# Performance work log

Hardware: AMD Instinct MI355X
Metric: run time of the kernel (lower is better)

## Reference

```python
import jax, jax.numpy as jnp
import numpy as np

B, S, D = 4, 8192, 768
H, HD = 12, 64
CS, NL = 512, 32


def setup_inputs() -> dict:
    key = jax.random.key(0)
    ks = jax.random.split(key, 9)
    sc = 0.02
    return {
        "x": jax.random.normal(ks[0], (B, S, D), jnp.float32),
        "q_w": jax.random.normal(ks[1], (D, D), jnp.float32) * sc,
        "q_b": jax.random.normal(ks[2], (D,), jnp.float32) * sc,
        "k_w": jax.random.normal(ks[3], (D, D), jnp.float32) * sc,
        "k_b": jax.random.normal(ks[4], (D,), jnp.float32) * sc,
        "v_w": jax.random.normal(ks[5], (D, D), jnp.float32) * sc,
        "v_b": jax.random.normal(ks[6], (D,), jnp.float32) * sc,
        "o_w": jax.random.normal(ks[7], (D, D), jnp.float32) * sc,
        "o_b": jax.random.normal(ks[8], (D,), jnp.float32) * sc,
    }


def reference(x, q_w, q_b, k_w, k_b, v_w, v_b, o_w, o_b):
    # x: (B, S, D); S divisible by CS and NL -> no padding / trimming needed.
    scale = HD ** -0.5
    n_chunks = S // CS
    seg = S // NL
    # Global landmarks: mean-pool NL evenly spaced segments. (B, NL, D)
    landmarks = x.reshape(B, NL, seg, D).mean(axis=2)
    # Q only over local tokens (torch Linear: x @ W^T + b)
    q = (x @ q_w.T + q_b).reshape(B, n_chunks, CS, H, HD)
    x_chunks = x.reshape(B, n_chunks, CS, D)
    # Prepend landmarks to every chunk's KV context: ctx = NL + CS
    lm = jnp.broadcast_to(landmarks[:, None], (B, n_chunks, NL, D))
    kv_ctx = jnp.concatenate([lm, x_chunks], axis=2)  # (B, n_chunks, ctx, D)
    ctx = NL + CS
    k = (kv_ctx @ k_w.T + k_b).reshape(B, n_chunks, ctx, H, HD)
    v = (kv_ctx @ v_w.T + v_b).reshape(B, n_chunks, ctx, H, HD)
    scores = jnp.einsum("bnqhd,bnkhd->bnhqk", q, k) * scale
    attn = jax.nn.softmax(scores, axis=-1)  # dropout=0 (eval)
    out = jnp.einsum("bnhqk,bnkhd->bnqhd", attn, v).reshape(B, S, D)
    return out @ o_w.T + o_b
```

## Files before the change

### kernel.cpp

```cpp
#include <hip/hip_runtime.h>


typedef unsigned short u16;
typedef __attribute__((ext_vector_type(8))) short short8;
typedef __attribute__((ext_vector_type(8))) unsigned short u16x8;
typedef __attribute__((ext_vector_type(4))) float f32x4;

__device__ __forceinline__ u16 f2bf(float f) {
    unsigned u = __float_as_uint(f);
    u += 0x7fffu + ((u >> 16) & 1u);
    return (u16)(u >> 16);
}

#define MFMA_BF16(A, B, C) __builtin_amdgcn_mfma_f32_16x16x32_bf16((A), (B), (C), 0, 0, 0)

__device__ __forceinline__ void gload16(const u16* g, const short* l) {
    __builtin_amdgcn_global_load_lds(
        (__attribute__((address_space(1))) void*)g,
        (__attribute__((address_space(3))) void*)l, 16, 0, 0);
}

__global__ __launch_bounds__(256) void k_cvtx(const float* __restrict__ x,
                                              u16* __restrict__ xa,
                                              float* __restrict__ part) {
    const int g = blockIdx.x;
    const int t = threadIdx.x;
    const float* base = x + (size_t)g * 64 * 768;
    u16* ob = xa + (size_t)g * 64 * 768;
    float s0 = 0.f, s1 = 0.f, s2 = 0.f;
    for (int r = 0; r < 64; ++r) {
        const size_t off = (size_t)r * 768;
        const float v0 = base[off + t], v1 = base[off + t + 256], v2 = base[off + t + 512];
        s0 += v0; s1 += v1; s2 += v2;
        ob[off + t] = f2bf(v0); ob[off + t + 256] = f2bf(v1); ob[off + t + 512] = f2bf(v2);
    }
    float* p = part + (size_t)g * 768;
    p[t] = s0; p[t + 256] = s1; p[t + 512] = s2;
}

__global__ void k_lmred(const float* __restrict__ part, u16* __restrict__ xa_lm) {
    const int bl = blockIdx.x;
    const int t = threadIdx.x;
    const float* p = part + (size_t)bl * 4 * 768;
    const float inv = 1.f / 256.f;
    for (int c = t; c < 768; c += 256) {
        const float s = p[c] + p[768 + c] + p[1536 + c] + p[2304 + c];
        xa_lm[(size_t)bl * 768 + c] = f2bf(s * inv);
    }
}

__global__ void k_cvtw(const float* __restrict__ qw, const float* __restrict__ kw,
                       const float* __restrict__ vw, const float* __restrict__ ow,
                       const float* __restrict__ qb, const float* __restrict__ kb,
                       const float* __restrict__ vb,
                       u16* __restrict__ wcat, u16* __restrict__ owb,
                       float* __restrict__ bcat) {
    const int yy = blockIdx.y;
    const int i = blockIdx.x * 256 + threadIdx.x;
    if (yy == 4) {
        if (i < 768)       bcat[i] = qb[i];
        else if (i < 1536) bcat[i] = kb[i - 768];
        else if (i < 2304) bcat[i] = vb[i - 1536];
        return;
    }
    const float* src = (yy == 0) ? qw : (yy == 1) ? kw : (yy == 2) ? vw : ow;
    u16* dst = (yy == 3) ? owb : wcat + (size_t)yy * 589824;
    const float4 v = ((const float4*)src)[i];
    ushort4 o;
    o.x = f2bf(v.x); o.y = f2bf(v.y); o.z = f2bf(v.z); o.w = f2bf(v.w);
    ((ushort4*)dst)[i] = o;
}

template <int MODE>
__global__ __launch_bounds__(256) void k_gemm(
    const u16* __restrict__ A, const u16* __restrict__ Bw, const float* __restrict__ bias,
    u16* __restrict__ q, u16* __restrict__ ktok, u16* __restrict__ vtok,
    u16* __restrict__ klm, u16* __restrict__ vlm, float* __restrict__ outf)
{
    __shared__ short lA[128 * 64];
    __shared__ short lB[128 * 64];
    const int t = threadIdx.x;
    const int wid = t >> 6, l = t & 63, lr = l & 15, lg = l >> 4;
    const int wm = wid >> 1, wn = wid & 1;

    const int gx = gridDim.x;
    const int nwg = gx * gridDim.y;
    const int orig = blockIdx.x + gx * blockIdx.y;
    const int qq = nwg >> 3, rr = nwg & 7, xcd = orig & 7, ii = orig >> 3;
    const int wg = (xcd < rr ? xcd * (qq + 1) : rr * (qq + 1) + (xcd - rr) * qq) + ii;
    const int m0 = (wg / gx) * 128, n0 = (wg % gx) * 128;

    const int srow = t >> 3;
    const int scol = (t & 7) * 8;
    const u16* ga = A  + (size_t)(m0 + srow) * 768 + scol;
    const u16* gb = Bw + (size_t)(n0 + srow) * 768 + scol;
    const int lbase = wid * 8 * 64;

    f32x4 acc[4][4] = {};

    for (int kt = 0; kt < 12; ++kt) {
        const int k0 = kt * 64;
        __syncthreads();
#pragma unroll
        for (int i = 0; i < 4; ++i) {
            gload16(ga + (size_t)(i * 32) * 768 + k0, &lA[i * 32 * 64 + lbase]);
            gload16(gb + (size_t)(i * 32) * 768 + k0, &lB[i * 32 * 64 + lbase]);
        }
        __syncthreads();
#pragma unroll
        for (int kf = 0; kf < 2; ++kf) {
            short8 af[4], bf2[4];
#pragma unroll
            for (int x = 0; x < 4; ++x) {
                af[x]  = *(const short8*)&lA[(wm * 64 + x * 16 + lr) * 64 + kf * 32 + lg * 8];
                bf2[x] = *(const short8*)&lB[(wn * 64 + x * 16 + lr) * 64 + kf * 32 + lg * 8];
            }
#pragma unroll
            for (int mf = 0; mf < 4; ++mf)
#pragma unroll
                for (int nf = 0; nf < 4; ++nf)
                    acc[mf][nf] = MFMA_BF16(af[mf], bf2[nf], acc[mf][nf]);
        }
    }

    if (MODE == 0) {
        const bool is_lm = (m0 >= 32768);
#pragma unroll
        for (int nf = 0; nf < 4; ++nf) {
            const int gn = n0 + wn * 64 + nf * 16 + lr;
            const float bv = bias[gn];
            const int region = gn / 768;
            const int nn = gn - region * 768;
            const int h = nn >> 6, d = nn & 63;
            u16* dst  = (region == 0) ? q : (region == 1) ? ktok : vtok;
            u16* dstl = (region == 1) ? klm : vlm;
#pragma unroll
            for (int mf = 0; mf < 4; ++mf) {
                const int gmb = m0 + wm * 64 + mf * 16 + lg * 4;
#pragma unroll
                for (int r = 0; r < 4; ++r) {
                    const u16 val = f2bf(acc[mf][nf][r] + bv);
                    const int gm = gmb + r;
                    if (!is_lm) {
                        const int b = gm >> 13, s = gm & 8191;
                        dst[((size_t)(b * 12 + h) * 8192 + s) * 64 + d] = val;
                    } else if (region > 0) {
                        const int ii2 = gm - 32768;
                        const int b = ii2 >> 5, lmr = ii2 & 31;
                        dstl[((size_t)(b * 12 + h) * 32 + lmr) * 64 + d] = val;
                    }
                }
            }
        }
    } else {
#pragma unroll
        for (int nf = 0; nf < 4; ++nf) {
            const int gn = n0 + wn * 64 + nf * 16 + lr;
            const float bv = bias[gn];
#pragma unroll
            for (int mf = 0; mf < 4; ++mf) {
                const int gmb = m0 + wm * 64 + mf * 16 + lg * 4;
#pragma unroll
                for (int r = 0; r < 4; ++r)
                    outf[(size_t)(gmb + r) * 768 + gn] = acc[mf][nf][r] + bv;
            }
        }
    }
}

__global__ __launch_bounds__(256) void k_tv(const u16* __restrict__ vtok, u16* __restrict__ vt) {
    __shared__ u16 tl[64 * 72];
    const int t = threadIdx.x;
    const int bh = blockIdx.x >> 7;
    const int s0 = (blockIdx.x & 127) * 64;
#pragma unroll
    for (int i = 0; i < 2; ++i) {
        const int qq = t + 256 * i;
        const int s = qq >> 3, c = qq & 7;
        *(uint4*)&tl[s * 72 + c * 8] =
            *(const uint4*)(vtok + ((size_t)bh * 8192 + s0 + s) * 64 + c * 8);
    }
    __syncthreads();
    const int d = t >> 2, sc = t & 3;
    u16x8 a, b2;
#pragma unroll
    for (int j = 0; j < 8; ++j) a[j] = tl[(sc * 16 + j) * 72 + d];
#pragma unroll
    for (int j = 0; j < 8; ++j) b2[j] = tl[(sc * 16 + 8 + j) * 72 + d];
    u16* o = vt + ((size_t)bh * 64 + d) * 8192 + s0 + sc * 16;
    *(u16x8*)(o) = a;
    *(u16x8*)(o + 8) = b2;
}

__global__ void k_tvlm(const u16* __restrict__ vlm, u16* __restrict__ vlmt) {
    const int e = blockIdx.x * 256 + threadIdx.x;
    if (e >= 98304) return;
    const int bh = e >> 11, rem = e & 2047, d = rem >> 5, lm = rem & 31;
    vlmt[(size_t)bh * 2048 + d * 32 + lm] = vlm[(size_t)bh * 2048 + lm * 64 + d];
}

__global__ __launch_bounds__(256) void k_attn(
    const u16* __restrict__ q, const u16* __restrict__ ktok,
    const u16* __restrict__ klm, const u16* __restrict__ vt,
    const u16* __restrict__ vlmt, u16* __restrict__ ao)
{
    __shared__ short kls[2][32 * 72];
    __shared__ short vls[2][64 * 40];
    __shared__ short pls[4][64 * 40];
    const int t = threadIdx.x, wid = t >> 6, l = t & 63, lr = l & 15, lg = l >> 4;
    const int idx = blockIdx.x;
    const int qt = idx & 1;
    const int h  = (idx >> 1) % 12;
    const int cb = (idx >> 1) / 12;
    const int c  = cb & 15, b = cb >> 4;
    const int bh = b * 12 + h;
    const int sb = c * 512 + qt * 256 + wid * 64;

    short8 qf[4][2];
#pragma unroll
    for (int mf = 0; mf < 4; ++mf)
#pragma unroll
        for (int kf = 0; kf < 2; ++kf)
            qf[mf][kf] = *(const short8*)(q + ((size_t)bh * 8192 + sb + mf * 16 + lr) * 64
                                            + kf * 32 + lg * 8);

    f32x4 O[4][4] = {};
    float lsum[4][4] = {};

    short* pw = &pls[wid][0];
    const int kn = t >> 3, kko = (t & 7) * 8;
    const int kctx = (kn < 16) ? (kn * 2) : ((kn - 16) * 2 + 1);
    const int vd = t >> 2, vco = (t & 3) * 8;

    auto kaddr = [&](int ti) -> const u16* {
        if (ti == 0) return klm + ((size_t)bh * 32 + kctx) * 64 + kko;
        return ktok + ((size_t)bh * 8192 + c * 512 + (ti - 1) * 32 + kctx) * 64 + kko;
    };
    auto vaddr = [&](int ti) -> const u16* {
        if (ti == 0) return vlmt + ((size_t)bh * 64 + vd) * 32 + vco;
        return vt + ((size_t)bh * 64 + vd) * 8192 + c * 512 + (ti - 1) * 32 + vco;
    };

    {
        const uint4 rk0 = *(const uint4*)kaddr(0);
        const uint4 rv0 = *(const uint4*)vaddr(0);
        *(uint4*)&kls[0][kn * 72 + kko] = rk0;
        *(uint4*)&vls[0][vd * 40 + vco] = rv0;
    }
    __syncthreads();

    for (int ti = 0; ti < 17; ++ti) {
        const int cur = ti & 1, nxt = cur ^ 1;
        uint4 rk, rv;
        if (ti < 16) { rk = *(const uint4*)kaddr(ti + 1); rv = *(const uint4*)vaddr(ti + 1); }

        f32x4 sc[4][2] = {};
#pragma unroll
        for (int kf = 0; kf < 2; ++kf) {
            const short8 b0 = *(const short8*)&kls[cur][(lr)      * 72 + kf * 32 + lg * 8];
            const short8 b1 = *(const short8*)&kls[cur][(16 + lr) * 72 + kf * 32 + lg * 8];
#pragma unroll
            for (int mf = 0; mf < 4; ++mf) {
                sc[mf][0] = MFMA_BF16(qf[mf][kf], b0, sc[mf][0]);
                sc[mf][1] = MFMA_BF16(qf[mf][kf], b1, sc[mf][1]);
            }
        }

#pragma unroll
        for (int mf = 0; mf < 4; ++mf) {
#pragma unroll
            for (int r = 0; r < 4; ++r) {
                const float p0 = __expf(sc[mf][0][r] * 0.125f);
                const float p1 = __expf(sc[mf][1][r] * 0.125f);
                lsum[mf][r] += p0 + p1;
                unsigned pk;
                asm("v_cvt_pk_bf16_f32 %0, %1, %2" : "=v"(pk) : "v"(p0), "v"(p1));
                const int prow = mf * 16 + lg * 4 + r;
                ((unsigned*)pw)[prow * 20 + lr] = pk;
            }
        }

        short8 vb[4];
#pragma unroll
        for (int df = 0; df < 4; ++df)
            vb[df] = *(const short8*)&vls[cur][(df * 16 + lr) * 40 + lg * 8];
#pragma unroll
        for (int mf = 0; mf < 4; ++mf) {
            const short8 pa = *(const short8*)&pw[(mf * 16 + lr) * 40 + lg * 8];
#pragma unroll
            for (int df = 0; df < 4; ++df)
                O[mf][df] = MFMA_BF16(pa, vb[df], O[mf][df]);
        }

        if (ti < 16) {
            *(uint4*)&kls[nxt][kn * 72 + kko] = rk;
            *(uint4*)&vls[nxt][vd * 40 + vco] = rv;
        }
        __syncthreads();
    }

#pragma unroll
    for (int mf = 0; mf < 4; ++mf)
#pragma unroll
        for (int r = 0; r < 4; ++r) {
            float lv = lsum[mf][r];
            lv += __shfl_xor(lv, 1); lv += __shfl_xor(lv, 2);
            lv += __shfl_xor(lv, 4); lv += __shfl_xor(lv, 8);
            const float inv = 1.f / lv;
            const int srow = sb + mf * 16 + lg * 4 + r;
#pragma unroll
            for (int df = 0; df < 4; ++df)
                ao[((size_t)b * 8192 + srow) * 768 + h * 64 + df * 16 + lr] =
                    f2bf(O[mf][df][r] * inv);
        }
}

extern "C" void kernel_launch(void* const* d_in, const int* in_sizes, int n_in,
                              void* d_out, int out_size, void* d_ws, size_t ws_size,
                              hipStream_t stream)
{
    const float* x  = (const float*)d_in[0];
    const float* qw = (const float*)d_in[1];
    const float* qb = (const float*)d_in[2];
    const float* kw = (const float*)d_in[3];
    const float* kb = (const float*)d_in[4];
    const float* vw = (const float*)d_in[5];
    const float* vb = (const float*)d_in[6];
    const float* ow = (const float*)d_in[7];
    const float* ob = (const float*)d_in[8];
    float* out = (float*)d_out;

    u16* xa     = (u16*)d_ws;
    u16* wcat   = xa + (size_t)32896 * 768;
    u16* owb    = wcat + (size_t)2304 * 768;
    float* bcat = (float*)(owb + (size_t)768 * 768);
    u16* qx     = (u16*)(bcat + 2304);
    u16* ktok   = qx   + (size_t)32768 * 768;
    u16* vtok   = ktok + (size_t)32768 * 768;
    u16* vt     = vtok + (size_t)32768 * 768;
    u16* klm    = vt + (size_t)32768 * 768;
    u16* vlm    = klm + 98304;
    u16* vlmt   = vlm + 98304;
    float* part = (float*)(vlmt + 98304);
    u16* ao     = xa;

    k_cvtx<<<512, 256, 0, stream>>>(x, xa, part);
    k_lmred<<<128, 256, 0, stream>>>(part, xa + (size_t)32768 * 768);
    k_cvtw<<<dim3(576, 5), 256, 0, stream>>>(qw, kw, vw, ow, qb, kb, vb, wcat, owb, bcat);

    k_gemm<0><<<dim3(18, 257), 256, 0, stream>>>(xa, wcat, bcat,
                                                 qx, ktok, vtok, klm, vlm, nullptr);
    k_tv<<<6144, 256, 0, stream>>>(vtok, vt);
    k_tvlm<<<384, 256, 0, stream>>>(vlm, vlmt);
    k_attn<<<1536, 256, 0, stream>>>(qx, ktok, klm, vt, vlmt, ao);
    k_gemm<1><<<dim3(6, 256), 256, 0, stream>>>(ao, owb, ob,
                                                nullptr, nullptr, nullptr, nullptr, nullptr, out);
}
```

Before: 431.5 us.

## Rewrite GEMM as 256x256 tiles with 4-stage async LDS pipeline and 8 waves

The QKV and output projection GEMM kernel moves from 128x128 tiles with 4 waves and a single-buffered, fully synchronised K loop to 256x256 tiles with 8 waves. It uses a 4-deep ring of LDS buffers filled by direct global-to-LDS loads three steps ahead, with explicit vmcnt waits and s_setprio around the MFMA bursts. This is meant to hide global load latency and raise arithmetic intensity per tile. In exchange it uses much more LDS (128 KB per block), so occupancy drops. Row clamping and bounds checks are added for the partial landmark tile.

```diff
diff --git a/kernel.cpp b/kernel.cpp
--- a/kernel.cpp
+++ b/kernel.cpp
@@ -72,94 +72,114 @@
 }
 
 template <int MODE>
-__global__ __launch_bounds__(256) void k_gemm(
+__global__ __launch_bounds__(512, 2) void k_gemm(
     const u16* __restrict__ A, const u16* __restrict__ Bw, const float* __restrict__ bias,
     u16* __restrict__ q, u16* __restrict__ ktok, u16* __restrict__ vtok,
     u16* __restrict__ klm, u16* __restrict__ vlm, float* __restrict__ outf)
 {
-    __shared__ short lA[128 * 64];
-    __shared__ short lB[128 * 64];
+    __shared__ short lA[4 * 8192];
+    __shared__ short lB[4 * 8192];
     const int t = threadIdx.x;
-    const int wid = t >> 6, l = t & 63, lr = l & 15, lg = l >> 4;
-    const int wm = wid >> 1, wn = wid & 1;
+    const int wid = t >> 6, lane = t & 63, lr = lane & 15, lg = lane >> 4;
+    const int wm = wid >> 2, wn = wid & 3;
 
     const int gx = gridDim.x;
     const int nwg = gx * gridDim.y;
     const int orig = blockIdx.x + gx * blockIdx.y;
     const int qq = nwg >> 3, rr = nwg & 7, xcd = orig & 7, ii = orig >> 3;
     const int wg = (xcd < rr ? xcd * (qq + 1) : rr * (qq + 1) + (xcd - rr) * qq) + ii;
-    const int m0 = (wg / gx) * 128, n0 = (wg % gx) * 128;
-
-    const int srow = t >> 3;
-    const int scol = (t & 7) * 8;
-    const u16* ga = A  + (size_t)(m0 + srow) * 768 + scol;
-    const u16* gb = Bw + (size_t)(n0 + srow) * 768 + scol;
-    const int lbase = wid * 8 * 64;
-
-    f32x4 acc[4][4] = {};
-
-    for (int kt = 0; kt < 12; ++kt) {
-        const int k0 = kt * 64;
-        __syncthreads();
-#pragma unroll
-        for (int i = 0; i < 4; ++i) {
-            gload16(ga + (size_t)(i * 32) * 768 + k0, &lA[i * 32 * 64 + lbase]);
-            gload16(gb + (size_t)(i * 32) * 768 + k0, &lB[i * 32 * 64 + lbase]);
-        }
-        __syncthreads();
-#pragma unroll
-        for (int kf = 0; kf < 2; ++kf) {
-            short8 af[4], bf2[4];
-#pragma unroll
-            for (int x = 0; x < 4; ++x) {
-                af[x]  = *(const short8*)&lA[(wm * 64 + x * 16 + lr) * 64 + kf * 32 + lg * 8];
-                bf2[x] = *(const short8*)&lB[(wn * 64 + x * 16 + lr) * 64 + kf * 32 + lg * 8];
+    const int m0 = (wg / gx) * 256, n0 = (wg % gx) * 256;
+
+    const int MMAX = (MODE == 0) ? 32895 : 32767;
+    const int i0 = t, i1 = 512 + t;
+    int ra0 = m0 + (i0 >> 2); if (ra0 > MMAX) ra0 = MMAX;
+    int ra1 = m0 + (i1 >> 2); if (ra1 > MMAX) ra1 = MMAX;
+    const u16* gA0 = A  + (size_t)ra0 * 768 + (i0 & 3) * 8;
+    const u16* gA1 = A  + (size_t)ra1 * 768 + (i1 & 3) * 8;
+    const u16* gB0 = Bw + (size_t)(n0 + (i0 >> 2)) * 768 + (i0 & 3) * 8;
+    const u16* gB1 = Bw + (size_t)(n0 + (i1 >> 2)) * 768 + (i1 & 3) * 8;
+    const int sd0 = wid * 512;
+    const int sd1 = 4096 + wid * 512;
+
+#define STAGE(TT) { const int sb_ = ((TT) & 3) * 8192; const int ks_ = (TT) * 32;      \
+    gload16(gA0 + ks_, &lA[sb_ + sd0]); gload16(gA1 + ks_, &lA[sb_ + sd1]);            \
+    gload16(gB0 + ks_, &lB[sb_ + sd0]); gload16(gB1 + ks_, &lB[sb_ + sd1]); }
+
+    f32x4 acc[8][4] = {};
+    STAGE(0); STAGE(1); STAGE(2);
+
+    for (int tt = 0; tt < 24; ++tt) {
+        if (tt < 22)       asm volatile("s_waitcnt vmcnt(8)" ::: "memory");
+        else if (tt == 22) asm volatile("s_waitcnt vmcnt(4)" ::: "memory");
+        else               asm volatile("s_waitcnt vmcnt(0)" ::: "memory");
+        __builtin_amdgcn_s_barrier();
+        __builtin_amdgcn_sched_barrier(0);
+        if (tt + 3 < 24) STAGE(tt + 3);
+
+        const short* sa = &lA[(tt & 3) * 8192];
+        const short* sb = &lB[(tt & 3) * 8192];
+        short8 bfr[4], afr[4];
+#pragma unroll
+        for (int nf = 0; nf < 4; ++nf)
+            bfr[nf] = *(const short8*)&sb[(wn * 64 + nf * 16 + lr) * 32 + lg * 8];
+#pragma unroll
+        for (int mf = 0; mf < 4; ++mf)
+            afr[mf] = *(const short8*)&sa[(wm * 128 + mf * 16 + lr) * 32 + lg * 8];
+        __builtin_amdgcn_s_setprio(1);
+#pragma unroll
+        for (int mf = 0; mf < 4; ++mf)
+#pragma unroll
+            for (int nf = 0; nf < 4; ++nf)
+                acc[mf][nf] = MFMA_BF16(afr[mf], bfr[nf], acc[mf][nf]);
+        __builtin_amdgcn_s_setprio(0);
+#pragma unroll
+        for (int mf = 0; mf < 4; ++mf)
+            afr[mf] = *(const short8*)&sa[(wm * 128 + (mf + 4) * 16 + lr) * 32 + lg * 8];
+        __builtin_amdgcn_s_setprio(1);
+#pragma unroll
+        for (int mf = 0; mf < 4; ++mf)
+#pragma unroll
+            for (int nf = 0; nf < 4; ++nf)
+                acc[mf + 4][nf] = MFMA_BF16(afr[mf], bfr[nf], acc[mf + 4][nf]);
+        __builtin_amdgcn_s_setprio(0);
+    }
+#undef STAGE
+
+    if (MODE == 0) {
+        const int region = n0 / 768;
+        u16* dst  = (region == 0) ? q : (region == 1) ? ktok : vtok;
+        u16* dstl = (region == 1) ? klm : vlm;
+#pragma unroll
+        for (int nf = 0; nf < 4; ++nf) {
+            const int gn = n0 + wn * 64 + nf * 16 + lr;
+            const int nn = gn - region * 768;
+            const int h = nn >> 6, d = nn & 63;
+            const float bv = bias[gn];
+#pragma unroll
+            for (int mf = 0; mf < 8; ++mf) {
+                const int gmb = m0 + wm * 128 + mf * 16 + lg * 4;
+#pragma unroll
+                for (int r = 0; r < 4; ++r) {
+                    const int gm = gmb + r;
+                    const u16 val = f2bf(acc[mf][nf][r] + bv);
+                    if (gm < 32768) {
+                        const int b = gm >> 13, s = gm & 8191;
+                        dst[((size_t)(b * 12 + h) * 8192 + s) * 64 + d] = val;
+                    } else if (gm < 32896 && region > 0) {
+                        const int ii2 = gm - 32768;
+                        dstl[((size_t)((ii2 >> 5) * 12 + h) * 32 + (ii2 & 31)) * 64 + d] = val;
+                    }
+                }
             }
-#pragma unroll
-            for (int mf = 0; mf < 4; ++mf)
-#pragma unroll
-                for (int nf = 0; nf < 4; ++nf)
-                    acc[mf][nf] = MFMA_BF16(af[mf], bf2[nf], acc[mf][nf]);
-        }
-    }
-
-    if (MODE == 0) {
-        const bool is_lm = (m0 >= 32768);
+        }
+    } else {
 #pragma unroll
         for (int nf = 0; nf < 4; ++nf) {
             const int gn = n0 + wn * 64 + nf * 16 + lr;
             const float bv = bias[gn];
-            const int region = gn / 768;
-            const int nn = gn - region * 768;
-            const int h = nn >> 6, d = nn & 63;
-            u16* dst  = (region == 0) ? q : (region == 1) ? ktok : vtok;
-            u16* dstl = (region == 1) ? klm : vlm;
-#pragma unroll
-            for (int mf = 0; mf < 4; ++mf) {
-                const int gmb = m0 + wm * 64 + mf * 16 + lg * 4;
-#pragma unroll
-                for (int r = 0; r < 4; ++r) {
-                    const u16 val = f2bf(acc[mf][nf][r] + bv);
-                    const int gm = gmb + r;
-                    if (!is_lm) {
-                        const int b = gm >> 13, s = gm & 8191;
-                        dst[((size_t)(b * 12 + h) * 8192 + s) * 64 + d] = val;
-                    } else if (region > 0) {
-                        const int ii2 = gm - 32768;
-                        const int b = ii2 >> 5, lmr = ii2 & 31;
-                        dstl[((size_t)(b * 12 + h) * 32 + lmr) * 64 + d] = val;
-                    }
-                }
-            }
-        }
-    } else {
-#pragma unroll
-        for (int nf = 0; nf < 4; ++nf) {
-            const int gn = n0 + wn * 64 + nf * 16 + lr;
-            const float bv = bias[gn];
-#pragma unroll
-            for (int mf = 0; mf < 4; ++mf) {
-                const int gmb = m0 + wm * 64 + mf * 16 + lg * 4;
+#pragma unroll
+            for (int mf = 0; mf < 8; ++mf) {
+                const int gmb = m0 + wm * 128 + mf * 16 + lg * 4;
 #pragma unroll
                 for (int r = 0; r < 4; ++r)
                     outf[(size_t)(gmb + r) * 768 + gn] = acc[mf][nf][r] + bv;
@@ -348,11 +368,11 @@
     k_lmred<<<128, 256, 0, stream>>>(part, xa + (size_t)32768 * 768);
     k_cvtw<<<dim3(576, 5), 256, 0, stream>>>(qw, kw, vw, ow, qb, kb, vb, wcat, owb, bcat);
 
-    k_gemm<0><<<dim3(18, 257), 256, 0, stream>>>(xa, wcat, bcat,
-                                                 qx, ktok, vtok, klm, vlm, nullptr);
+    k_gemm<0><<<dim3(9, 129), 512, 0, stream>>>(xa, wcat, bcat,
+                                                qx, ktok, vtok, klm, vlm, nullptr);
     k_tv<<<6144, 256, 0, stream>>>(vtok, vt);
     k_tvlm<<<384, 256, 0, stream>>>(vlm, vlmt);
     k_attn<<<1536, 256, 0, stream>>>(qx, ktok, klm, vt, vlmt, ao);
-    k_gemm<1><<<dim3(6, 256), 256, 0, stream>>>(ao, owb, ob,
+    k_gemm<1><<<dim3(3, 128), 512, 0, stream>>>(ao, owb, ob,
                                                 nullptr, nullptr, nullptr, nullptr, nullptr, out);
 }
```

Result: slower. 468.1 us (+8.5%).
